# Kernel tuning notes

Hardware: AMD Instinct MI355X
Metric: run time of the kernel (lower is better)

Reference implementation:

```python
import jax, jax.numpy as jnp
import numpy as np

NUM_HEADS = 32

def setup_inputs() -> dict:
    key = jax.random.key(0)
    k1, k2, k3 = jax.random.split(key, 3)
    B, C, H, W = 4, 768, 32, 32
    x = jax.random.normal(k1, (B, C, H, W), dtype=jnp.float32)
    # 1x1 conv kernels represented as [C_in, C_out] matrices
    w_qkv = jax.random.normal(k2, (C, 3 * C), dtype=jnp.float32) * (2.0 / (3 * C)) ** 0.5
    b_qkv = jnp.zeros((3 * C,), dtype=jnp.float32)
    w_proj = jax.random.normal(k3, (C, C), dtype=jnp.float32) * (2.0 / C) ** 0.5
    b_proj = jnp.zeros((C,), dtype=jnp.float32)
    return {"x": x, "w_qkv": w_qkv, "b_qkv": b_qkv, "w_proj": w_proj, "b_proj": b_proj}

def reference(x, w_qkv, b_qkv, w_proj, b_proj):
    B, C, H, W = x.shape
    h = NUM_HEADS
    hd = C // h
    scale = hd ** (-0.5)
    # qkv 1x1 conv (channels_first): [B,C,H,W] -> [B,3C,H,W]
    qkv = jnp.einsum('bchw,cd->bdhw', x, w_qkv) + b_qkv[None, :, None, None]
    qkv = qkv.reshape(B, 3, h, hd, H * W)
    q = qkv[:, 0]  # [B,h,hd,HW]
    k = qkv[:, 1]  # [B,h,hd,HW]
    v = qkv[:, 2]  # [B,h,hd,HW]
    # attn = q^T @ k : [B,h,HW,HW]
    attn = jnp.einsum('bhdq,bhdk->bhqk', q, k) * scale
    attn = jax.nn.softmax(attn, axis=-1)
    # out = (attn @ v^T)^T : [B,h,hd,HW]
    o = jnp.einsum('bhqk,bhdk->bhdq', attn, v)
    o = o.reshape(B, C, H, W)
    # proj 1x1 conv
    out = jnp.einsum('bchw,cf->bfhw', o, w_proj) + b_proj[None, :, None, None]
    return out
```

## Files before the change

kernel.cpp:

```cpp
#include <hip/hip_runtime.h>
#include <hip/hip_bf16.h>

#define B_  4
#define C_  768
#define N_  1024
#define NH  32
#define HD  24
#define HDP 32
#define D3  2304
#define QSCALE 0.29448889f

typedef __hip_bfloat16 bf16;
typedef __attribute__((ext_vector_type(8))) short bf16x8;
typedef __attribute__((ext_vector_type(4))) float f32x4;

__device__ __forceinline__ unsigned cvt_pk_bf16(float lo, float hi) {
    unsigned r;
    asm volatile("v_cvt_pk_bf16_f32 %0, %1, %2" : "=v"(r) : "v"(lo), "v"(hi));
    return r;
}

__device__ __forceinline__ float fast_exp2(float x) {
    float r;
    asm volatile("v_exp_f32 %0, %1" : "=v"(r) : "v"(x));
    return r;
}

__device__ __forceinline__ void gload_lds16(const bf16* g, bf16* l) {
    __builtin_amdgcn_global_load_lds(
        (const __attribute__((address_space(1))) void*)g,
        (__attribute__((address_space(3))) void*)l, 16, 0, 0);
}

__global__ __launch_bounds__(256) void prep(
        const float* __restrict__ x, const float* __restrict__ w_qkv,
        const float* __restrict__ w_proj,
        bf16* __restrict__ xt, bf16* __restrict__ wqT, bf16* __restrict__ wpT,
        bf16* __restrict__ vB) {
    const int bid = blockIdx.x;
    if (bid >= 5376) {
        const int head = bid - 5376;
        bf16* row = vB + ((size_t)head * HDP + 24) * N_;
        const ushort4 ones = {0x3F80, 0x3F80, 0x3F80, 0x3F80};
        *(ushort4*)&row[threadIdx.x * 4] = ones;
        return;
    }
    const float* src; bf16* dst; int R, Cc, r0, c0;
    if (bid < 3072) {
        const int b = bid / 768, rem = bid % 768;
        R = 768; Cc = 1024;
        src = x + (size_t)b * 768 * 1024;
        dst = xt + (size_t)b * 1024 * 768;
        c0 = (rem % 32) * 32; r0 = (rem / 32) * 32;
    } else if (bid < 4800) {
        const int rem = bid - 3072;
        R = 768; Cc = 2304; src = w_qkv; dst = wqT;
        c0 = (rem % 72) * 32; r0 = (rem / 72) * 32;
    } else {
        const int rem = bid - 4800;
        R = 768; Cc = 768; src = w_proj; dst = wpT;
        c0 = (rem % 24) * 32; r0 = (rem / 24) * 32;
    }
    __shared__ float tile[32][33];
    const int tx = threadIdx.x & 31, ty = threadIdx.x >> 5;
    #pragma unroll
    for (int k = 0; k < 4; k++)
        tile[ty + 8*k][tx] = src[(size_t)(r0 + ty + 8*k) * Cc + c0 + tx];
    __syncthreads();
    #pragma unroll
    for (int k = 0; k < 4; k++)
        dst[(size_t)(c0 + ty + 8*k) * R + r0 + tx] = __float2bfloat16(tile[tx][ty + 8*k]);
}

__global__ __launch_bounds__(256) void gemm_qkv(
        const bf16* __restrict__ xt, const bf16* __restrict__ wqT,
        const float* __restrict__ bqkv,
        bf16* __restrict__ qT, bf16* __restrict__ kT, bf16* __restrict__ vB) {
    __shared__ bf16 As[2][64 * 32];
    __shared__ bf16 Bs[2][128 * 32];

    const int bid = blockIdx.x;
    const bool vmode = (bid >= 768);
    const bf16* Ap; const bf16* Bp; int M0, Nc0;
    if (!vmode) {
        Ap = xt;                       Bp = wqT;
        M0 = (bid & 63) * 64;          Nc0 = (bid >> 6) * 128;
    } else {
        const int r = bid - 768;
        Ap = wqT + (size_t)1536 * C_;  Bp = xt;
        M0 = (r % 12) * 64;            Nc0 = (r / 12) * 128;
    }

    const int t = threadIdx.x;
    const int lane = t & 63, wid = t >> 6;
    const int c = lane & 15, g = lane >> 4;
    const int wm = wid >> 1, wn = wid & 1;

    const int srow = lane >> 2, schunk = lane & 3;
    const bf16* AgP = Ap + (size_t)(M0 + wid * 16 + srow) * C_ + schunk * 8;
    const bf16* Bg0 = Bp + (size_t)(Nc0 + wid * 32 + srow) * C_ + schunk * 8;
    const bf16* Bg1 = Bg0 + 16 * C_;

    f32x4 acc[2][4];
    #pragma unroll
    for (int i = 0; i < 2; i++)
        #pragma unroll
        for (int j = 0; j < 4; j++) acc[i][j] = f32x4{0.f, 0.f, 0.f, 0.f};

    gload_lds16(AgP, &As[0][(wid * 16) * 32]);
    gload_lds16(Bg0, &Bs[0][(wid * 32) * 32]);
    gload_lds16(Bg1, &Bs[0][(wid * 32 + 16) * 32]);
    __syncthreads();

    int cur = 0;
    for (int s = 0; s < 24; s++) {
        if (s < 23) {
            const int k1 = (s + 1) * 32;
            gload_lds16(AgP + k1, &As[cur ^ 1][(wid * 16) * 32]);
            gload_lds16(Bg0 + k1, &Bs[cur ^ 1][(wid * 32) * 32]);
            gload_lds16(Bg1 + k1, &Bs[cur ^ 1][(wid * 32 + 16) * 32]);
        }
        bf16x8 af[2], bfr[4];
        #pragma unroll
        for (int mi = 0; mi < 2; mi++)
            af[mi] = *(const bf16x8*)&As[cur][(wm * 32 + mi * 16 + c) * 32 + g * 8];
        #pragma unroll
        for (int ni = 0; ni < 4; ni++)
            bfr[ni] = *(const bf16x8*)&Bs[cur][(wn * 64 + ni * 16 + c) * 32 + g * 8];
        #pragma unroll
        for (int mi = 0; mi < 2; mi++)
            #pragma unroll
            for (int ni = 0; ni < 4; ni++)
                acc[mi][ni] = __builtin_amdgcn_mfma_f32_16x16x32_bf16(
                    af[mi], bfr[ni], acc[mi][ni], 0, 0, 0);
        __syncthreads();
        cur ^= 1;
    }

    const int row0 = M0 + wm * 32, col0 = Nc0 + wn * 64;
    if (!vmode) {
        #pragma unroll
        for (int ni = 0; ni < 4; ni++) {
            const int j = col0 + ni * 16 + c;
            const int issec = j >= 768;
            bf16* dstbase = issec ? kT : qT;
            const int dd = j - (issec ? 768 : 0);
            const int hh = dd / 24, hd = dd % 24;
            const float bq = bqkv[j];
            const float sca = issec ? 1.0f : QSCALE;
            #pragma unroll
            for (int mi = 0; mi < 2; mi++)
                #pragma unroll
                for (int r = 0; r < 4; r++) {
                    const int n = row0 + mi * 16 + 4 * g + r;
                    const int b = n >> 10, nn = n & 1023;
                    dstbase[(((size_t)(b * NH + hh) * N_) + nn) * HDP + hd] =
                        __float2bfloat16((acc[mi][ni][r] + bq) * sca);
                }
        }
    } else {
        #pragma unroll
        for (int mi = 0; mi < 2; mi++)
            #pragma unroll
            for (int r = 0; r < 4; r++) {
                const int vd = row0 + mi * 16 + 4 * g + r;
                const int hh = vd / 24, hd = vd % 24;
                const float bq = bqkv[1536 + vd];
                #pragma unroll
                for (int ni = 0; ni < 4; ni++) {
                    const int n = col0 + ni * 16 + c;
                    const int b = n >> 10, nn = n & 1023;
                    vB[((size_t)(b * NH + hh) * HDP + hd) * N_ + nn] =
                        __float2bfloat16(acc[mi][ni][r] + bq);
                }
            }
    }
}

__global__ __launch_bounds__(256) void gemm_proj(
        const bf16* __restrict__ wpT, const bf16* __restrict__ obuf,
        const float* __restrict__ bproj, float* __restrict__ outF) {
    __shared__ bf16 As[2][64 * 32];
    __shared__ bf16 Bs[2][128 * 32];

    const int b = blockIdx.z;
    const bf16* Ap = wpT;
    const bf16* Bp = obuf + (size_t)b * N_ * C_;
    const int M0 = blockIdx.x * 64, Nc0 = blockIdx.y * 128;

    const int t = threadIdx.x;
    const int lane = t & 63, wid = t >> 6;
    const int c = lane & 15, g = lane >> 4;
    const int wm = wid >> 1, wn = wid & 1;

    const int srow = lane >> 2, schunk = lane & 3;
    const bf16* AgP = Ap + (size_t)(M0 + wid * 16 + srow) * C_ + schunk * 8;
    const bf16* Bg0 = Bp + (size_t)(Nc0 + wid * 32 + srow) * C_ + schunk * 8;
    const bf16* Bg1 = Bg0 + 16 * C_;

    f32x4 acc[2][4];
    #pragma unroll
    for (int i = 0; i < 2; i++)
        #pragma unroll
        for (int j = 0; j < 4; j++) acc[i][j] = f32x4{0.f, 0.f, 0.f, 0.f};

    gload_lds16(AgP, &As[0][(wid * 16) * 32]);
    gload_lds16(Bg0, &Bs[0][(wid * 32) * 32]);
    gload_lds16(Bg1, &Bs[0][(wid * 32 + 16) * 32]);
    __syncthreads();

    int cur = 0;
    for (int s = 0; s < 24; s++) {
        if (s < 23) {
            const int k1 = (s + 1) * 32;
            gload_lds16(AgP + k1, &As[cur ^ 1][(wid * 16) * 32]);
            gload_lds16(Bg0 + k1, &Bs[cur ^ 1][(wid * 32) * 32]);
            gload_lds16(Bg1 + k1, &Bs[cur ^ 1][(wid * 32 + 16) * 32]);
        }
        bf16x8 af[2], bfr[4];
        #pragma unroll
        for (int mi = 0; mi < 2; mi++)
            af[mi] = *(const bf16x8*)&As[cur][(wm * 32 + mi * 16 + c) * 32 + g * 8];
        #pragma unroll
        for (int ni = 0; ni < 4; ni++)
            bfr[ni] = *(const bf16x8*)&Bs[cur][(wn * 64 + ni * 16 + c) * 32 + g * 8];
        #pragma unroll
        for (int mi = 0; mi < 2; mi++)
            #pragma unroll
            for (int ni = 0; ni < 4; ni++)
                acc[mi][ni] = __builtin_amdgcn_mfma_f32_16x16x32_bf16(
                    af[mi], bfr[ni], acc[mi][ni], 0, 0, 0);
        __syncthreads();
        cur ^= 1;
    }

    const int row0 = M0 + wm * 32, col0 = Nc0 + wn * 64;
    #pragma unroll
    for (int mi = 0; mi < 2; mi++)
        #pragma unroll
        for (int r = 0; r < 4; r++) {
            const int f = row0 + mi * 16 + 4 * g + r;
            const float bp = bproj[f];
            #pragma unroll
            for (int ni = 0; ni < 4; ni++) {
                const int n = col0 + ni * 16 + c;
                outF[((size_t)b * C_ + f) * N_ + n] = acc[mi][ni][r] + bp;
            }
        }
}

__global__ __launch_bounds__(256) void attn_mfma(
        const bf16* __restrict__ qT, const bf16* __restrict__ kT,
        const bf16* __restrict__ vB, bf16* __restrict__ obuf) {
    __shared__ bf16 Kb[2][64 * 40];
    __shared__ bf16 Vb[2][32 * 72];
    __shared__ bf16 Ps[4][32 * 72];

    const int t = threadIdx.x, lane = t & 63, wid = t >> 6;
    const int c = lane & 15, g = lane >> 4;
    const int bid = blockIdx.x;
    const int xcd = bid & 7, idx = bid >> 3;
    const int hl = xcd * 16 + (idx & 15);
    const int qb = idx >> 4;
    const int b = hl >> 5, h = hl & 31;
    const int q0 = qb * 128 + wid * 32;
    const size_t hb = (size_t)(b * NH + h);
    const bf16* qh = qT + hb * N_ * HDP;
    const bf16* kh = kT + hb * N_ * HDP;
    const bf16* vh = vB + hb * HDP * N_;
    bf16* myPs = &Ps[wid][0];

    bf16x8 qf0 = *(const bf16x8*)(qh + (size_t)(q0 + c) * HDP + g * 8);
    bf16x8 qf1 = *(const bf16x8*)(qh + (size_t)(q0 + 16 + c) * HDP + g * 8);
    if (g == 3) {
        const bf16x8 z8 = {0, 0, 0, 0, 0, 0, 0, 0};
        qf0 = z8; qf1 = z8;
    }
    f32x4 o00 = {0.f,0.f,0.f,0.f}, o01 = {0.f,0.f,0.f,0.f};
    f32x4 o10 = {0.f,0.f,0.f,0.f}, o11 = {0.f,0.f,0.f,0.f};

    const bf16* kgp = kh + (size_t)(t >> 2) * HDP + (t & 3) * 8;
    const bf16* vgp = vh + (size_t)(t >> 3) * N_ + (t & 7) * 8;
    const int kws = (t >> 2) * 40 + (t & 3) * 8;
    const int vws = (t >> 3) * 72 + (t & 7) * 8;

    int4 rk = *(const int4*)kgp;
    int4 rv = *(const int4*)vgp;
    *(int4*)&Kb[0][kws] = rk;
    *(int4*)&Vb[0][vws] = rv;
    __syncthreads();

    int cur = 0;
    for (int kt = 0; kt < 16; kt++) {
        if (kt < 15) {
            const int k1 = (kt + 1) * 64;
            rk = *(const int4*)(kgp + (size_t)k1 * HDP);
            rv = *(const int4*)(vgp + k1);
        }
        f32x4 st0[4], st1[4];
        #pragma unroll
        for (int tt = 0; tt < 4; tt++) {
            bf16x8 kf = *(const bf16x8*)&Kb[cur][(tt * 16 + c) * 40 + g * 8];
            f32x4 z = {0.f, 0.f, 0.f, 0.f};
            st0[tt] = __builtin_amdgcn_mfma_f32_16x16x32_bf16(kf, qf0, z, 0, 0, 0);
            st1[tt] = __builtin_amdgcn_mfma_f32_16x16x32_bf16(kf, qf1, z, 0, 0, 0);
        }
        float p0[16], p1[16];
        #pragma unroll
        for (int tt = 0; tt < 4; tt++)
            #pragma unroll
            for (int r = 0; r < 4; r++) {
                p0[tt * 4 + r] = fast_exp2(st0[tt][r]);
                p1[tt * 4 + r] = fast_exp2(st1[tt][r]);
            }
        #pragma unroll
        for (int tt = 0; tt < 4; tt++) {
            uint2 w0, w1;
            w0.x = cvt_pk_bf16(p0[tt * 4 + 0], p0[tt * 4 + 1]);
            w0.y = cvt_pk_bf16(p0[tt * 4 + 2], p0[tt * 4 + 3]);
            w1.x = cvt_pk_bf16(p1[tt * 4 + 0], p1[tt * 4 + 1]);
            w1.y = cvt_pk_bf16(p1[tt * 4 + 2], p1[tt * 4 + 3]);
            *(uint2*)&myPs[c * 72 + tt * 16 + g * 4]        = w0;
            *(uint2*)&myPs[(16 + c) * 72 + tt * 16 + g * 4] = w1;
        }
        bf16x8 pa00 = *(const bf16x8*)&myPs[c * 72 + g * 8];
        bf16x8 pa01 = *(const bf16x8*)&myPs[c * 72 + 32 + g * 8];
        bf16x8 pa10 = *(const bf16x8*)&myPs[(16 + c) * 72 + g * 8];
        bf16x8 pa11 = *(const bf16x8*)&myPs[(16 + c) * 72 + 32 + g * 8];

        bf16x8 va0 = *(const bf16x8*)&Vb[cur][c * 72 + g * 8];
        bf16x8 va1 = *(const bf16x8*)&Vb[cur][c * 72 + 32 + g * 8];
        bf16x8 vb0 = *(const bf16x8*)&Vb[cur][(16 + c) * 72 + g * 8];
        bf16x8 vb1 = *(const bf16x8*)&Vb[cur][(16 + c) * 72 + 32 + g * 8];
        o00 = __builtin_amdgcn_mfma_f32_16x16x32_bf16(pa00, va0, o00, 0, 0, 0);
        o00 = __builtin_amdgcn_mfma_f32_16x16x32_bf16(pa01, va1, o00, 0, 0, 0);
        o01 = __builtin_amdgcn_mfma_f32_16x16x32_bf16(pa00, vb0, o01, 0, 0, 0);
        o01 = __builtin_amdgcn_mfma_f32_16x16x32_bf16(pa01, vb1, o01, 0, 0, 0);
        o10 = __builtin_amdgcn_mfma_f32_16x16x32_bf16(pa10, va0, o10, 0, 0, 0);
        o10 = __builtin_amdgcn_mfma_f32_16x16x32_bf16(pa11, va1, o10, 0, 0, 0);
        o11 = __builtin_amdgcn_mfma_f32_16x16x32_bf16(pa10, vb0, o11, 0, 0, 0);
        o11 = __builtin_amdgcn_mfma_f32_16x16x32_bf16(pa11, vb1, o11, 0, 0, 0);

        if (kt < 15) {
            *(int4*)&Kb[cur ^ 1][kws] = rk;
            *(int4*)&Vb[cur ^ 1][vws] = rv;
        }
        __syncthreads();
        cur ^= 1;
    }

    float inv0[4], inv1[4];
    #pragma unroll
    for (int r = 0; r < 4; r++) {
        inv0[r] = 1.f / __shfl(o01[r], g * 16 + 8);
        inv1[r] = 1.f / __shfl(o11[r], g * 16 + 8);
    }
    #pragma unroll
    for (int dt = 0; dt < 2; dt++) {
        const int dcol = dt * 16 + c;
        if (dcol < HD) {
            const f32x4 oa = dt ? o01 : o00;
            const f32x4 ob = dt ? o11 : o10;
            #pragma unroll
            for (int r = 0; r < 4; r++) {
                const int qa = q0 + g * 4 + r;
                const int qb2 = q0 + 16 + g * 4 + r;
                obuf[((size_t)b * N_ + qa) * C_ + h * HD + dcol] =
                    __float2bfloat16(oa[r] * inv0[r]);
                obuf[((size_t)b * N_ + qb2) * C_ + h * HD + dcol] =
                    __float2bfloat16(ob[r] * inv1[r]);
            }
        }
    }
}

extern "C" void kernel_launch(void* const* d_in, const int* in_sizes, int n_in,
                              void* d_out, int out_size, void* d_ws, size_t ws_size,
                              hipStream_t stream) {
    const float* x      = (const float*)d_in[0];
    const float* w_qkv  = (const float*)d_in[1];
    const float* b_qkv  = (const float*)d_in[2];
    const float* w_proj = (const float*)d_in[3];
    const float* b_proj = (const float*)d_in[4];
    float* out = (float*)d_out;

    char* ws = (char*)d_ws;
    bf16* xt   = (bf16*)(ws);
    bf16* wqT  = (bf16*)(ws + 6291456);
    bf16* wpT  = (bf16*)(ws + 9830400);
    bf16* qT   = (bf16*)(ws + 11010048);
    bf16* kT   = (bf16*)(ws + 19398656);
    bf16* vB   = (bf16*)(ws + 27787264);
    bf16* obuf = (bf16*)(ws + 36175872);

    prep<<<dim3(5504), 256, 0, stream>>>(x, w_qkv, w_proj, xt, wqT, wpT, vB);
    gemm_qkv<<<dim3(1152), 256, 0, stream>>>(xt, wqT, b_qkv, qT, kT, vB);
    attn_mfma<<<dim3(1024), 256, 0, stream>>>(qT, kT, vB, obuf);
    gemm_proj<<<dim3(12, 8, 4), 256, 0, stream>>>(wpT, obuf, b_proj, out);
}
```

Before: 166.0 us.

## Triple-buffer GEMM LDS pipeline with one barrier per step and XCD block swizzle

```diff
diff --git a/kernel.cpp b/kernel.cpp
--- a/kernel.cpp
+++ b/kernel.cpp
@@ -76,10 +76,11 @@
         const bf16* __restrict__ xt, const bf16* __restrict__ wqT,
         const float* __restrict__ bqkv,
         bf16* __restrict__ qT, bf16* __restrict__ kT, bf16* __restrict__ vB) {
-    __shared__ bf16 As[2][64 * 32];
-    __shared__ bf16 Bs[2][128 * 32];
-
-    const int bid = blockIdx.x;
+    __shared__ bf16 As[3][64 * 32];
+    __shared__ bf16 Bs[3][128 * 32];
+
+    const int bid0 = blockIdx.x;
+    const int bid = (bid0 & 7) * 144 + (bid0 >> 3);
     const bool vmode = (bid >= 768);
     const bf16* Ap; const bf16* Bp; int M0, Nc0;
     if (!vmode) {
@@ -107,34 +108,40 @@
         #pragma unroll
         for (int j = 0; j < 4; j++) acc[i][j] = f32x4{0.f, 0.f, 0.f, 0.f};
 
-    gload_lds16(AgP, &As[0][(wid * 16) * 32]);
-    gload_lds16(Bg0, &Bs[0][(wid * 32) * 32]);
-    gload_lds16(Bg1, &Bs[0][(wid * 32 + 16) * 32]);
-    __syncthreads();
-
-    int cur = 0;
+    gload_lds16(AgP,          &As[0][(wid * 16) * 32]);
+    gload_lds16(Bg0,          &Bs[0][(wid * 32) * 32]);
+    gload_lds16(Bg1,          &Bs[0][(wid * 32 + 16) * 32]);
+    gload_lds16(AgP + 32,     &As[1][(wid * 16) * 32]);
+    gload_lds16(Bg0 + 32,     &Bs[1][(wid * 32) * 32]);
+    gload_lds16(Bg1 + 32,     &Bs[1][(wid * 32 + 16) * 32]);
+
+    #pragma unroll 3
     for (int s = 0; s < 24; s++) {
-        if (s < 23) {
-            const int k1 = (s + 1) * 32;
-            gload_lds16(AgP + k1, &As[cur ^ 1][(wid * 16) * 32]);
-            gload_lds16(Bg0 + k1, &Bs[cur ^ 1][(wid * 32) * 32]);
-            gload_lds16(Bg1 + k1, &Bs[cur ^ 1][(wid * 32 + 16) * 32]);
-        }
+        if (s < 23) asm volatile("s_waitcnt vmcnt(3)" ::: "memory");
+        else        asm volatile("s_waitcnt vmcnt(0)" ::: "memory");
+        __builtin_amdgcn_s_barrier();
+        __builtin_amdgcn_sched_barrier(0);
+        if (s + 2 < 24) {
+            const int k1 = (s + 2) * 32;
+            const int nb = (s + 2) % 3;
+            gload_lds16(AgP + k1, &As[nb][(wid * 16) * 32]);
+            gload_lds16(Bg0 + k1, &Bs[nb][(wid * 32) * 32]);
+            gload_lds16(Bg1 + k1, &Bs[nb][(wid * 32 + 16) * 32]);
+        }
+        const int cb = s % 3;
         bf16x8 af[2], bfr[4];
         #pragma unroll
         for (int mi = 0; mi < 2; mi++)
-            af[mi] = *(const bf16x8*)&As[cur][(wm * 32 + mi * 16 + c) * 32 + g * 8];
+            af[mi] = *(const bf16x8*)&As[cb][(wm * 32 + mi * 16 + c) * 32 + g * 8];
         #pragma unroll
         for (int ni = 0; ni < 4; ni++)
-            bfr[ni] = *(const bf16x8*)&Bs[cur][(wn * 64 + ni * 16 + c) * 32 + g * 8];
+            bfr[ni] = *(const bf16x8*)&Bs[cb][(wn * 64 + ni * 16 + c) * 32 + g * 8];
         #pragma unroll
         for (int mi = 0; mi < 2; mi++)
             #pragma unroll
             for (int ni = 0; ni < 4; ni++)
                 acc[mi][ni] = __builtin_amdgcn_mfma_f32_16x16x32_bf16(
                     af[mi], bfr[ni], acc[mi][ni], 0, 0, 0);
-        __syncthreads();
-        cur ^= 1;
     }
 
     const int row0 = M0 + wm * 32, col0 = Nc0 + wn * 64;
@@ -180,8 +187,8 @@
 __global__ __launch_bounds__(256) void gemm_proj(
         const bf16* __restrict__ wpT, const bf16* __restrict__ obuf,
         const float* __restrict__ bproj, float* __restrict__ outF) {
-    __shared__ bf16 As[2][64 * 32];
-    __shared__ bf16 Bs[2][128 * 32];
+    __shared__ bf16 As[3][64 * 32];
+    __shared__ bf16 Bs[3][128 * 32];
 
     const int b = blockIdx.z;
     const bf16* Ap = wpT;
@@ -204,34 +211,40 @@
         #pragma unroll
         for (int j = 0; j < 4; j++) acc[i][j] = f32x4{0.f, 0.f, 0.f, 0.f};
 
-    gload_lds16(AgP, &As[0][(wid * 16) * 32]);
-    gload_lds16(Bg0, &Bs[0][(wid * 32) * 32]);
-    gload_lds16(Bg1, &Bs[0][(wid * 32 + 16) * 32]);
-    __syncthreads();
-
-    int cur = 0;
+    gload_lds16(AgP,      &As[0][(wid * 16) * 32]);
+    gload_lds16(Bg0,      &Bs[0][(wid * 32) * 32]);
+    gload_lds16(Bg1,      &Bs[0][(wid * 32 + 16) * 32]);
+    gload_lds16(AgP + 32, &As[1][(wid * 16) * 32]);
+    gload_lds16(Bg0 + 32, &Bs[1][(wid * 32) * 32]);
+    gload_lds16(Bg1 + 32, &Bs[1][(wid * 32 + 16) * 32]);
+
+    #pragma unroll 3
     for (int s = 0; s < 24; s++) {
-        if (s < 23) {
-            const int k1 = (s + 1) * 32;
-            gload_lds16(AgP + k1, &As[cur ^ 1][(wid * 16) * 32]);
-            gload_lds16(Bg0 + k1, &Bs[cur ^ 1][(wid * 32) * 32]);
-            gload_lds16(Bg1 + k1, &Bs[cur ^ 1][(wid * 32 + 16) * 32]);
-        }
+        if (s < 23) asm volatile("s_waitcnt vmcnt(3)" ::: "memory");
+        else        asm volatile("s_waitcnt vmcnt(0)" ::: "memory");
+        __builtin_amdgcn_s_barrier();
+        __builtin_amdgcn_sched_barrier(0);
+        if (s + 2 < 24) {
+            const int k1 = (s + 2) * 32;
+            const int nb = (s + 2) % 3;
+            gload_lds16(AgP + k1, &As[nb][(wid * 16) * 32]);
+            gload_lds16(Bg0 + k1, &Bs[nb][(wid * 32) * 32]);
+            gload_lds16(Bg1 + k1, &Bs[nb][(wid * 32 + 16) * 32]);
+        }
+        const int cb = s % 3;
         bf16x8 af[2], bfr[4];
         #pragma unroll
         for (int mi = 0; mi < 2; mi++)
-            af[mi] = *(const bf16x8*)&As[cur][(wm * 32 + mi * 16 + c) * 32 + g * 8];
+            af[mi] = *(const bf16x8*)&As[cb][(wm * 32 + mi * 16 + c) * 32 + g * 8];
         #pragma unroll
         for (int ni = 0; ni < 4; ni++)
-            bfr[ni] = *(const bf16x8*)&Bs[cur][(wn * 64 + ni * 16 + c) * 32 + g * 8];
+            bfr[ni] = *(const bf16x8*)&Bs[cb][(wn * 64 + ni * 16 + c) * 32 + g * 8];
         #pragma unroll
         for (int mi = 0; mi < 2; mi++)
             #pragma unroll
             for (int ni = 0; ni < 4; ni++)
                 acc[mi][ni] = __builtin_amdgcn_mfma_f32_16x16x32_bf16(
                     af[mi], bfr[ni], acc[mi][ni], 0, 0, 0);
-        __syncthreads();
-        cur ^= 1;
     }
 
     const int row0 = M0 + wm * 32, col0 = Nc0 + wn * 64;
```

Measured after the change: 161.3 us. -2.8%, faster.

## Register-prefetch GEMM pipelines, swizzle block order for XCDs, raise MFMA priority

Applied to the files above, without the earlier changes.

```diff
diff --git a/kernel.cpp b/kernel.cpp
--- a/kernel.cpp
+++ b/kernel.cpp
@@ -24,12 +24,6 @@
     float r;
     asm volatile("v_exp_f32 %0, %1" : "=v"(r) : "v"(x));
     return r;
-}
-
-__device__ __forceinline__ void gload_lds16(const bf16* g, bf16* l) {
-    __builtin_amdgcn_global_load_lds(
-        (const __attribute__((address_space(1))) void*)g,
-        (__attribute__((address_space(3))) void*)l, 16, 0, 0);
 }
 
 __global__ __launch_bounds__(256) void prep(
@@ -79,7 +73,8 @@
     __shared__ bf16 As[2][64 * 32];
     __shared__ bf16 Bs[2][128 * 32];
 
-    const int bid = blockIdx.x;
+    const int bid0 = blockIdx.x;
+    const int bid = (bid0 & 7) * 144 + (bid0 >> 3);
     const bool vmode = (bid >= 768);
     const bf16* Ap; const bf16* Bp; int M0, Nc0;
     if (!vmode) {
@@ -96,10 +91,12 @@
     const int c = lane & 15, g = lane >> 4;
     const int wm = wid >> 1, wn = wid & 1;
 
-    const int srow = lane >> 2, schunk = lane & 3;
-    const bf16* AgP = Ap + (size_t)(M0 + wid * 16 + srow) * C_ + schunk * 8;
-    const bf16* Bg0 = Bp + (size_t)(Nc0 + wid * 32 + srow) * C_ + schunk * 8;
-    const bf16* Bg1 = Bg0 + 16 * C_;
+    const int srow = t >> 2, schunk = (t & 3) * 8;
+    const bf16* Ag  = Ap + (size_t)(M0 + srow) * C_ + schunk;
+    const bf16* Bga = Bp + (size_t)(Nc0 + srow) * C_ + schunk;
+    const bf16* Bgb = Bga + (size_t)64 * C_;
+    const int aws = srow * 32 + schunk;
+    const int bws = srow * 32 + schunk;
 
     f32x4 acc[2][4];
     #pragma unroll
@@ -107,34 +104,48 @@
         #pragma unroll
         for (int j = 0; j < 4; j++) acc[i][j] = f32x4{0.f, 0.f, 0.f, 0.f};
 
-    gload_lds16(AgP, &As[0][(wid * 16) * 32]);
-    gload_lds16(Bg0, &Bs[0][(wid * 32) * 32]);
-    gload_lds16(Bg1, &Bs[0][(wid * 32 + 16) * 32]);
+    int4 ra  = *(const int4*)Ag;
+    int4 rb0 = *(const int4*)Bga;
+    int4 rb1 = *(const int4*)Bgb;
+    *(int4*)&As[0][aws] = ra;
+    *(int4*)&Bs[0][bws] = rb0;
+    *(int4*)&Bs[0][bws + 64 * 32] = rb1;
+    ra  = *(const int4*)(Ag + 32);
+    rb0 = *(const int4*)(Bga + 32);
+    rb1 = *(const int4*)(Bgb + 32);
     __syncthreads();
 
-    int cur = 0;
+    #pragma unroll 2
     for (int s = 0; s < 24; s++) {
-        if (s < 23) {
-            const int k1 = (s + 1) * 32;
-            gload_lds16(AgP + k1, &As[cur ^ 1][(wid * 16) * 32]);
-            gload_lds16(Bg0 + k1, &Bs[cur ^ 1][(wid * 32) * 32]);
-            gload_lds16(Bg1 + k1, &Bs[cur ^ 1][(wid * 32 + 16) * 32]);
-        }
+        const int cb = s & 1;
         bf16x8 af[2], bfr[4];
         #pragma unroll
         for (int mi = 0; mi < 2; mi++)
-            af[mi] = *(const bf16x8*)&As[cur][(wm * 32 + mi * 16 + c) * 32 + g * 8];
+            af[mi] = *(const bf16x8*)&As[cb][(wm * 32 + mi * 16 + c) * 32 + g * 8];
         #pragma unroll
         for (int ni = 0; ni < 4; ni++)
-            bfr[ni] = *(const bf16x8*)&Bs[cur][(wn * 64 + ni * 16 + c) * 32 + g * 8];
+            bfr[ni] = *(const bf16x8*)&Bs[cb][(wn * 64 + ni * 16 + c) * 32 + g * 8];
+        __builtin_amdgcn_s_setprio(1);
         #pragma unroll
         for (int mi = 0; mi < 2; mi++)
             #pragma unroll
             for (int ni = 0; ni < 4; ni++)
                 acc[mi][ni] = __builtin_amdgcn_mfma_f32_16x16x32_bf16(
                     af[mi], bfr[ni], acc[mi][ni], 0, 0, 0);
-        __syncthreads();
-        cur ^= 1;
+        __builtin_amdgcn_s_setprio(0);
+        if (s < 23) {
+            __syncthreads();
+            *(int4*)&As[cb ^ 1][aws] = ra;
+            *(int4*)&Bs[cb ^ 1][bws] = rb0;
+            *(int4*)&Bs[cb ^ 1][bws + 64 * 32] = rb1;
+            if (s < 22) {
+                const int k1 = (s + 2) * 32;
+                ra  = *(const int4*)(Ag + k1);
+                rb0 = *(const int4*)(Bga + k1);
+                rb1 = *(const int4*)(Bgb + k1);
+            }
+            __syncthreads();
+        }
     }
 
     const int row0 = M0 + wm * 32, col0 = Nc0 + wn * 64;
@@ -183,20 +194,25 @@
     __shared__ bf16 As[2][64 * 32];
     __shared__ bf16 Bs[2][128 * 32];
 
-    const int b = blockIdx.z;
+    const int bid0 = blockIdx.x;
+    const int bid = (bid0 & 7) * 48 + (bid0 >> 3);
+    const int mt = bid % 12, rem = bid / 12;
+    const int nt = rem & 7, b = rem >> 3;
     const bf16* Ap = wpT;
     const bf16* Bp = obuf + (size_t)b * N_ * C_;
-    const int M0 = blockIdx.x * 64, Nc0 = blockIdx.y * 128;
+    const int M0 = mt * 64, Nc0 = nt * 128;
 
     const int t = threadIdx.x;
     const int lane = t & 63, wid = t >> 6;
     const int c = lane & 15, g = lane >> 4;
     const int wm = wid >> 1, wn = wid & 1;
 
-    const int srow = lane >> 2, schunk = lane & 3;
-    const bf16* AgP = Ap + (size_t)(M0 + wid * 16 + srow) * C_ + schunk * 8;
-    const bf16* Bg0 = Bp + (size_t)(Nc0 + wid * 32 + srow) * C_ + schunk * 8;
-    const bf16* Bg1 = Bg0 + 16 * C_;
+    const int srow = t >> 2, schunk = (t & 3) * 8;
+    const bf16* Ag  = Ap + (size_t)(M0 + srow) * C_ + schunk;
+    const bf16* Bga = Bp + (size_t)(Nc0 + srow) * C_ + schunk;
+    const bf16* Bgb = Bga + (size_t)64 * C_;
+    const int aws = srow * 32 + schunk;
+    const int bws = srow * 32 + schunk;
 
     f32x4 acc[2][4];
     #pragma unroll
@@ -204,34 +220,48 @@
         #pragma unroll
         for (int j = 0; j < 4; j++) acc[i][j] = f32x4{0.f, 0.f, 0.f, 0.f};
 
-    gload_lds16(AgP, &As[0][(wid * 16) * 32]);
-    gload_lds16(Bg0, &Bs[0][(wid * 32) * 32]);
-    gload_lds16(Bg1, &Bs[0][(wid * 32 + 16) * 32]);
+    int4 ra  = *(const int4*)Ag;
+    int4 rb0 = *(const int4*)Bga;
+    int4 rb1 = *(const int4*)Bgb;
+    *(int4*)&As[0][aws] = ra;
+    *(int4*)&Bs[0][bws] = rb0;
+    *(int4*)&Bs[0][bws + 64 * 32] = rb1;
+    ra  = *(const int4*)(Ag + 32);
+    rb0 = *(const int4*)(Bga + 32);
+    rb1 = *(const int4*)(Bgb + 32);
     __syncthreads();
 
-    int cur = 0;
+    #pragma unroll 2
     for (int s = 0; s < 24; s++) {
-        if (s < 23) {
-            const int k1 = (s + 1) * 32;
-            gload_lds16(AgP + k1, &As[cur ^ 1][(wid * 16) * 32]);
-            gload_lds16(Bg0 + k1, &Bs[cur ^ 1][(wid * 32) * 32]);
-            gload_lds16(Bg1 + k1, &Bs[cur ^ 1][(wid * 32 + 16) * 32]);
-        }
+        const int cb = s & 1;
         bf16x8 af[2], bfr[4];
         #pragma unroll
         for (int mi = 0; mi < 2; mi++)
-            af[mi] = *(const bf16x8*)&As[cur][(wm * 32 + mi * 16 + c) * 32 + g * 8];
+            af[mi] = *(const bf16x8*)&As[cb][(wm * 32 + mi * 16 + c) * 32 + g * 8];
         #pragma unroll
         for (int ni = 0; ni < 4; ni++)
-            bfr[ni] = *(const bf16x8*)&Bs[cur][(wn * 64 + ni * 16 + c) * 32 + g * 8];
+            bfr[ni] = *(const bf16x8*)&Bs[cb][(wn * 64 + ni * 16 + c) * 32 + g * 8];
+        __builtin_amdgcn_s_setprio(1);
         #pragma unroll
         for (int mi = 0; mi < 2; mi++)
             #pragma unroll
             for (int ni = 0; ni < 4; ni++)
                 acc[mi][ni] = __builtin_amdgcn_mfma_f32_16x16x32_bf16(
                     af[mi], bfr[ni], acc[mi][ni], 0, 0, 0);
-        __syncthreads();
-        cur ^= 1;
+        __builtin_amdgcn_s_setprio(0);
+        if (s < 23) {
+            __syncthreads();
+            *(int4*)&As[cb ^ 1][aws] = ra;
+            *(int4*)&Bs[cb ^ 1][bws] = rb0;
+            *(int4*)&Bs[cb ^ 1][bws + 64 * 32] = rb1;
+            if (s < 22) {
+                const int k1 = (s + 2) * 32;
+                ra  = *(const int4*)(Ag + k1);
+                rb0 = *(const int4*)(Bga + k1);
+                rb1 = *(const int4*)(Bgb + k1);
+            }
+            __syncthreads();
+        }
     }
 
     const int row0 = M0 + wm * 32, col0 = Nc0 + wn * 64;
@@ -298,6 +328,7 @@
             rv = *(const int4*)(vgp + k1);
         }
         f32x4 st0[4], st1[4];
+        __builtin_amdgcn_s_setprio(1);
         #pragma unroll
         for (int tt = 0; tt < 4; tt++) {
             bf16x8 kf = *(const bf16x8*)&Kb[cur][(tt * 16 + c) * 40 + g * 8];
@@ -305,6 +336,7 @@
             st0[tt] = __builtin_amdgcn_mfma_f32_16x16x32_bf16(kf, qf0, z, 0, 0, 0);
             st1[tt] = __builtin_amdgcn_mfma_f32_16x16x32_bf16(kf, qf1, z, 0, 0, 0);
         }
+        __builtin_amdgcn_s_setprio(0);
         float p0[16], p1[16];
         #pragma unroll
         for (int tt = 0; tt < 4; tt++)
@@ -332,6 +364,7 @@
         bf16x8 va1 = *(const bf16x8*)&Vb[cur][c * 72 + 32 + g * 8];
         bf16x8 vb0 = *(const bf16x8*)&Vb[cur][(16 + c) * 72 + g * 8];
         bf16x8 vb1 = *(const bf16x8*)&Vb[cur][(16 + c) * 72 + 32 + g * 8];
+        __builtin_amdgcn_s_setprio(1);
         o00 = __builtin_amdgcn_mfma_f32_16x16x32_bf16(pa00, va0, o00, 0, 0, 0);
         o00 = __builtin_amdgcn_mfma_f32_16x16x32_bf16(pa01, va1, o00, 0, 0, 0);
         o01 = __builtin_amdgcn_mfma_f32_16x16x32_bf16(pa00, vb0, o01, 0, 0, 0);
@@ -340,6 +373,7 @@
         o10 = __builtin_amdgcn_mfma_f32_16x16x32_bf16(pa11, va1, o10, 0, 0, 0);
         o11 = __builtin_amdgcn_mfma_f32_16x16x32_bf16(pa10, vb0, o11, 0, 0, 0);
         o11 = __builtin_amdgcn_mfma_f32_16x16x32_bf16(pa11, vb1, o11, 0, 0, 0);
+        __builtin_amdgcn_s_setprio(0);
 
         if (kt < 15) {
             *(int4*)&Kb[cur ^ 1][kws] = rk;
@@ -396,5 +430,5 @@
     prep<<<dim3(5504), 256, 0, stream>>>(x, w_qkv, w_proj, xt, wqT, wpT, vB);
     gemm_qkv<<<dim3(1152), 256, 0, stream>>>(xt, wqT, b_qkv, qT, kT, vB);
     attn_mfma<<<dim3(1024), 256, 0, stream>>>(qT, kT, vB, obuf);
-    gemm_proj<<<dim3(12, 8, 4), 256, 0, stream>>>(wpT, obuf, b_proj, out);
-}
+    gemm_proj<<<dim3(384), 256, 0, stream>>>(wpT, obuf, b_proj, out);
+}
```

After: 156.4 us. -5.8%, faster.
